# Optimization experiments

Measured on AMD Instinct MI355X. Metric: run time of the kernel, lower is better.

Reference implementation:

```python
import jax, jax.numpy as jnp
import numpy as np

B, IN, H, U = 65536, 128, 256, 256

def lecun_tanh(x):
    return 1.7159 * jnp.tanh(0.666 * x)

def _xavier(key, shape):
    fan_out, fan_in = shape
    limit = np.sqrt(6.0 / (fan_in + fan_out))
    return jax.random.uniform(key, shape, jnp.float32, -limit, limit)

def setup_inputs() -> dict:
    key = jax.random.key(0)
    ks = jax.random.split(key, 12)
    return {
        "input": jax.random.normal(ks[0], (B, IN), jnp.float32),
        "hx": jax.random.normal(ks[1], (B, H), jnp.float32),
        "ts": jax.random.uniform(ks[2], (B, 1), jnp.float32),
        # backbone Linear(IN+H -> U)
        "Wb": _xavier(ks[3], (U, IN + H)),
        "bb": jnp.zeros((U,), jnp.float32),
        # ff1, ff2, time_a, time_b: Linear(U -> H)
        "W1": _xavier(ks[4], (H, U)),
        "b1": jnp.zeros((H,), jnp.float32),
        "W2": _xavier(ks[5], (H, U)),
        "b2": jnp.zeros((H,), jnp.float32),
        "Wa": _xavier(ks[6], (H, U)),
        "ba": jnp.zeros((H,), jnp.float32),
        "Wt": _xavier(ks[7], (H, U)),
        "bt": jnp.zeros((H,), jnp.float32),
    }

def reference(input, hx, ts, Wb, bb, W1, b1, W2, b2, Wa, ba, Wt, bt):
    # x = cat([input, hx]) -> backbone MLP (1 layer, LeCun tanh)
    x = jnp.concatenate([input, hx], axis=1)          # [B, IN+H]
    x = lecun_tanh(x @ Wb.T + bb)                     # [B, U]
    ff1 = jnp.tanh(x @ W1.T + b1)                     # [B, H]
    ff2 = jnp.tanh(x @ W2.T + b2)
    t_a = x @ Wa.T + ba
    t_b = x @ Wt.T + bt
    t_interp = jax.nn.sigmoid(t_a * ts + t_b)         # ts broadcasts [B,1]
    new_hidden = ff1 * (1.0 - t_interp) + t_interp * ff2
    return new_hidden
```

## Files before the change

kernel.cpp:

```cpp
#include <hip/hip_runtime.h>

typedef float v4f __attribute__((ext_vector_type(4)));
typedef short v8s __attribute__((ext_vector_type(8)));

#define BM 64

__device__ __forceinline__ unsigned short f2bf(float f) {
    union { float f; unsigned u; } v; v.f = f;
    unsigned u = v.u;
    u += 0x7FFFu + ((u >> 16) & 1u);
    return (unsigned short)(u >> 16);
}

__device__ __forceinline__ unsigned cvt_pk_bf16(float lo, float hi) {
    unsigned r;
    asm("v_cvt_pk_bf16_f32 %0, %1, %2" : "=v"(r) : "v"(lo), "v"(hi));
    return r;
}

__device__ __forceinline__ void gload_lds16(const unsigned short* g, unsigned short* l) {
    __builtin_amdgcn_global_load_lds(
        (const __attribute__((address_space(1))) void*)(const void*)g,
        (__attribute__((address_space(3))) void*)(void*)l,
        16, 0, 0);
}

#define LDS_BARRIER() do {                                        \
    asm volatile("s_waitcnt lgkmcnt(0)" ::: "memory");            \
    __builtin_amdgcn_s_barrier();                                 \
    __builtin_amdgcn_sched_barrier(0);                            \
} while (0)

__device__ __forceinline__ float fast_exp2(float x) {
#if __has_builtin(__builtin_amdgcn_exp2f)
    return __builtin_amdgcn_exp2f(x);
#else
    return exp2f(x);
#endif
}
__device__ __forceinline__ float fast_rcp(float x) {
#if __has_builtin(__builtin_amdgcn_rcpf)
    return __builtin_amdgcn_rcpf(x);
#else
    return 1.0f / x;
#endif
}
__device__ __forceinline__ float fast_tanh(float y) {
    float t = fast_exp2(y * 2.885390081777927f);
    return (t - 1.0f) * fast_rcp(t + 1.0f);
}
__device__ __forceinline__ float fast_sigmoid(float z) {
    float t = fast_exp2(-1.4426950408889634f * z);
    return fast_rcp(1.0f + t);
}

__global__ void prep_pack(const float* __restrict__ Wb, const float* __restrict__ W1,
                          const float* __restrict__ W2, const float* __restrict__ Wa,
                          const float* __restrict__ Wt, unsigned short* __restrict__ ws)
{
    int e = blockIdx.x * 256 + threadIdx.x;
    if (e >= 360448) return;
    const float* src; int K; int base;
    if (e < 98304)       { src = Wb; K = 384; base = 0; }
    else if (e < 163840) { src = W1; K = 256; base = 98304; }
    else if (e < 229376) { src = W2; K = 256; base = 163840; }
    else if (e < 294912) { src = Wa; K = 256; base = 229376; }
    else                 { src = Wt; K = 256; base = 294912; }
    int le   = e - base;
    int j    = le & 7;
    int lane = (le >> 3) & 63;
    int tile = le >> 9;
    int kt   = K >> 5;
    int ks   = tile % kt;
    int nt   = tile / kt;
    int n = nt * 16 + (lane & 15);
    int k = ks * 32 + (lane >> 4) * 8 + j;
    ws[e] = f2bf(src[n * K + k]);
}

__global__ __launch_bounds__(256, 2) void cfc_fused(
    const float* __restrict__ xin, const float* __restrict__ hx,
    const float* __restrict__ ts,
    const float* __restrict__ bb, const float* __restrict__ b1,
    const float* __restrict__ b2, const float* __restrict__ ba,
    const float* __restrict__ bt,
    const unsigned short* __restrict__ wpk,
    float* __restrict__ out)
{
    __shared__ unsigned short lds[40960];
    const int tid  = threadIdx.x;
    const int lane = tid & 63;
    const int w    = tid >> 6;
    const int row0 = blockIdx.x * BM;

    auto STAGE = [&](int s) {
        unsigned short* wb = &lds[16384 + (s % 3) * 8192 + w * 2048];
        #pragma unroll
        for (int i = 0; i < 4; ++i) {
            size_t goff;
            if (s < 12) {
                goff = (size_t)((w * 4 + i) * 12 + s) * 512;
            } else {
                int s2 = s - 12, g = s2 >> 3, ks = s2 & 7;
                goff = 98304u + (size_t)i * 65536
                     + (size_t)((w * 4 + g) * 8 + ks) * 512;
            }
            gload_lds16(wpk + goff + (size_t)lane * 8, wb + i * 512);
        }
    };

    STAGE(0); STAGE(1);

    v4f acc[4][4];
    #pragma unroll
    for (int nt = 0; nt < 4; ++nt) {
        float bv = bb[w * 64 + nt * 16 + (lane & 15)];
        v4f bvv = {bv, bv, bv, bv};
        #pragma unroll
        for (int mt = 0; mt < 4; ++mt) acc[nt][mt] = bvv;
    }

    #pragma unroll 1
    for (int c = 0; c < 3; ++c) {
        const float* src = (c == 0) ? (xin + (size_t)row0 * 128)
                                    : (hx + (size_t)row0 * 256 + (c == 2 ? 128 : 0));
        const int srcld = (c == 0) ? 128 : 256;
        v4f stg[8];
        #pragma unroll
        for (int it = 0; it < 8; ++it) {
            int i  = tid + it * 256;
            int r  = i >> 5;
            int c4 = i & 31;
            stg[it] = *(reinterpret_cast<const v4f*>(src + (size_t)r * srcld) + c4);
        }
        LDS_BARRIER();
        #pragma unroll
        for (int it = 0; it < 8; ++it) {
            int i  = tid + it * 256;
            int r  = i >> 5;
            int c4 = i & 31;
            uint2 pk;
            pk.x = cvt_pk_bf16(stg[it][0], stg[it][1]);
            pk.y = cvt_pk_bf16(stg[it][2], stg[it][3]);
            int idx = (((r >> 4) * 4 + (c4 >> 3)) * 64 + ((c4 >> 1) & 3) * 16 + (r & 15)) * 8
                      + (c4 & 1) * 4;
            *reinterpret_cast<uint2*>(&lds[idx]) = pk;
        }
        LDS_BARRIER();

        #pragma unroll 1
        for (int ksl = 0; ksl < 4; ++ksl) {
            const int s = c * 4 + ksl;
            STAGE(s + 2);
            asm volatile("s_waitcnt vmcnt(8)" ::: "memory");
            v8s a[4];
            #pragma unroll
            for (int mt = 0; mt < 4; ++mt)
                a[mt] = *reinterpret_cast<const v8s*>(&lds[((mt*4 + ksl)*64 + lane)*8]);
            const unsigned short* wb = &lds[16384 + (s % 3) * 8192 + w * 2048];
            v8s bf[4];
            #pragma unroll
            for (int nt = 0; nt < 4; ++nt)
                bf[nt] = *reinterpret_cast<const v8s*>(wb + nt * 512 + lane * 8);
            #pragma unroll
            for (int nt = 0; nt < 4; ++nt)
                #pragma unroll
                for (int mt = 0; mt < 4; ++mt)
                    acc[nt][mt] = __builtin_amdgcn_mfma_f32_16x16x32_bf16(a[mt], bf[nt], acc[nt][mt], 0, 0, 0);
        }
    }

    float tsh[4][4];
    #pragma unroll
    for (int mt = 0; mt < 4; ++mt)
        #pragma unroll
        for (int r = 0; r < 4; ++r)
            tsh[mt][r] = ts[row0 + mt*16 + ((lane >> 4) << 2) + r];

    LDS_BARRIER();

    #pragma unroll
    for (int nt = 0; nt < 4; ++nt)
        #pragma unroll
        for (int mt = 0; mt < 4; ++mt)
            #pragma unroll
            for (int r = 0; r < 4; ++r) {
                float xv = 1.7159f * fast_tanh(0.666f * acc[nt][mt][r]);
                int idx = ((mt*8 + w*2 + (nt >> 1)) * 64
                           + ((nt & 1)*2 + ((lane >> 3) & 1)) * 16 + (lane >> 4)*4 + r) * 8
                          + (lane & 7);
                lds[idx] = f2bf(xv);
            }
    LDS_BARRIER();

    #pragma unroll 1
    for (int g = 0; g < 4; ++g) {
        const int n = w * 64 + g * 16 + (lane & 15);
        v4f a2[4][4];
        {
            float v1 = b1[n], v2 = b2[n], va = ba[n], vt = bt[n];
            v4f q1 = {v1,v1,v1,v1}, q2 = {v2,v2,v2,v2}, qa = {va,va,va,va}, qt = {vt,vt,vt,vt};
            #pragma unroll
            for (int mt = 0; mt < 4; ++mt) {
                a2[0][mt] = q1; a2[1][mt] = q2; a2[2][mt] = qa; a2[3][mt] = qt;
            }
        }
        #pragma unroll 1
        for (int ks = 0; ks < 8; ++ks) {
            const int s = 12 + g * 8 + ks;
            if (s <= 41) {
                STAGE(s + 2);
                asm volatile("s_waitcnt vmcnt(8)" ::: "memory");
            } else if (s == 42) {
                asm volatile("s_waitcnt vmcnt(4)" ::: "memory");
            } else {
                asm volatile("s_waitcnt vmcnt(0)" ::: "memory");
            }
            v8s a[4];
            #pragma unroll
            for (int mt = 0; mt < 4; ++mt)
                a[mt] = *reinterpret_cast<const v8s*>(&lds[((mt*8 + ks)*64 + lane)*8]);
            const unsigned short* wb = &lds[16384 + (s % 3) * 8192 + w * 2048];
            v8s bf[4];
            #pragma unroll
            for (int mat = 0; mat < 4; ++mat)
                bf[mat] = *reinterpret_cast<const v8s*>(wb + mat * 512 + lane * 8);
            #pragma unroll
            for (int mat = 0; mat < 4; ++mat)
                #pragma unroll
                for (int mt = 0; mt < 4; ++mt)
                    a2[mat][mt] = __builtin_amdgcn_mfma_f32_16x16x32_bf16(a[mt], bf[mat], a2[mat][mt], 0, 0, 0);
        }
        #pragma unroll
        for (int mt = 0; mt < 4; ++mt) {
            int rowb = row0 + mt*16 + ((lane >> 4) << 2);
            #pragma unroll
            for (int r = 0; r < 4; ++r) {
                float ff1 = fast_tanh(a2[0][mt][r]);
                float ff2 = fast_tanh(a2[1][mt][r]);
                float ti  = fast_sigmoid(a2[2][mt][r] * tsh[mt][r] + a2[3][mt][r]);
                out[(size_t)(rowb + r) * 256 + n] = ff1 + ti * (ff2 - ff1);
            }
        }
    }
}

extern "C" void kernel_launch(void* const* d_in, const int* in_sizes, int n_in,
                              void* d_out, int out_size, void* d_ws, size_t ws_size,
                              hipStream_t stream)
{
    const float* xin = (const float*)d_in[0];
    const float* hx  = (const float*)d_in[1];
    const float* ts  = (const float*)d_in[2];
    const float* Wb  = (const float*)d_in[3];
    const float* bb  = (const float*)d_in[4];
    const float* W1  = (const float*)d_in[5];
    const float* b1  = (const float*)d_in[6];
    const float* W2  = (const float*)d_in[7];
    const float* b2  = (const float*)d_in[8];
    const float* Wa  = (const float*)d_in[9];
    const float* ba  = (const float*)d_in[10];
    const float* Wt  = (const float*)d_in[11];
    const float* bt  = (const float*)d_in[12];

    if (ws_size < 360448 * sizeof(unsigned short)) return;
    unsigned short* wpk = (unsigned short*)d_ws;

    prep_pack<<<1408, 256, 0, stream>>>(Wb, W1, W2, Wa, Wt, wpk);
    cfc_fused<<<1024, 256, 0, stream>>>(xin, hx, ts, bb, b1, b2, ba, bt, wpk,
                                        (float*)d_out);
}
```

Measured before the change: 79.09 us.

## Double-buffer LDS fragments in register for second GEMM and raise MFMA priority

The second GEMM loop now prefetches the next k-step's A and B fragments from LDS into a second set of registers while the current step's MFMAs run. To make that possible, the vmcnt wait is tightened so the following stage is already resident. In the first GEMM, A-fragment reads move ahead of the global-load wait. Both loops wrap their MFMA blocks in s_setprio to favour matrix issue across waves. The intent is to hide LDS read latency behind MFMA work, at the cost of more VGPRs and a tighter dependence on the global-to-LDS staging order.

```diff
diff --git a/kernel.cpp b/kernel.cpp
--- a/kernel.cpp
+++ b/kernel.cpp
@@ -152,21 +152,23 @@
         for (int ksl = 0; ksl < 4; ++ksl) {
             const int s = c * 4 + ksl;
             STAGE(s + 2);
-            asm volatile("s_waitcnt vmcnt(8)" ::: "memory");
             v8s a[4];
             #pragma unroll
             for (int mt = 0; mt < 4; ++mt)
                 a[mt] = *reinterpret_cast<const v8s*>(&lds[((mt*4 + ksl)*64 + lane)*8]);
+            asm volatile("s_waitcnt vmcnt(8)" ::: "memory");
             const unsigned short* wb = &lds[16384 + (s % 3) * 8192 + w * 2048];
             v8s bf[4];
             #pragma unroll
             for (int nt = 0; nt < 4; ++nt)
                 bf[nt] = *reinterpret_cast<const v8s*>(wb + nt * 512 + lane * 8);
+            __builtin_amdgcn_s_setprio(1);
             #pragma unroll
             for (int nt = 0; nt < 4; ++nt)
                 #pragma unroll
                 for (int mt = 0; mt < 4; ++mt)
                     acc[nt][mt] = __builtin_amdgcn_mfma_f32_16x16x32_bf16(a[mt], bf[nt], acc[nt][mt], 0, 0, 0);
+            __builtin_amdgcn_s_setprio(0);
         }
     }
 
@@ -192,6 +194,46 @@
                 lds[idx] = f2bf(xv);
             }
     LDS_BARRIER();
+
+    v8s afA[4], bfA[4], afB[4], bfB[4];
+
+    auto STEP = [&](v8s (&afC)[4], v8s (&bfC)[4], v8s (&afP)[4], v8s (&bfP)[4],
+                    v4f (&a2)[4][4], int g, int ks) {
+        const int s = 12 + g * 8 + ks;
+        if (s <= 41) {
+            STAGE(s + 2);
+            asm volatile("s_waitcnt vmcnt(4)" ::: "memory");
+        } else {
+            asm volatile("s_waitcnt vmcnt(0)" ::: "memory");
+        }
+        const int nks = (ks + 1) & 7;
+        const int sn  = (s < 43) ? (s + 1) : s;
+        #pragma unroll
+        for (int mt = 0; mt < 4; ++mt)
+            afP[mt] = *reinterpret_cast<const v8s*>(&lds[((mt*8 + nks)*64 + lane)*8]);
+        const unsigned short* wbp = &lds[16384 + (sn % 3) * 8192 + w * 2048];
+        #pragma unroll
+        for (int mat = 0; mat < 4; ++mat)
+            bfP[mat] = *reinterpret_cast<const v8s*>(wbp + mat * 512 + lane * 8);
+        __builtin_amdgcn_s_setprio(1);
+        #pragma unroll
+        for (int mat = 0; mat < 4; ++mat)
+            #pragma unroll
+            for (int mt = 0; mt < 4; ++mt)
+                a2[mat][mt] = __builtin_amdgcn_mfma_f32_16x16x32_bf16(afC[mt], bfC[mat], a2[mat][mt], 0, 0, 0);
+        __builtin_amdgcn_s_setprio(0);
+    };
+
+    asm volatile("s_waitcnt vmcnt(4)" ::: "memory");
+    #pragma unroll
+    for (int mt = 0; mt < 4; ++mt)
+        afA[mt] = *reinterpret_cast<const v8s*>(&lds[((mt*8 + 0)*64 + lane)*8]);
+    {
+        const unsigned short* wb = &lds[16384 + 0 * 8192 + w * 2048];
+        #pragma unroll
+        for (int mat = 0; mat < 4; ++mat)
+            bfA[mat] = *reinterpret_cast<const v8s*>(wb + mat * 512 + lane * 8);
+    }
 
     #pragma unroll 1
     for (int g = 0; g < 4; ++g) {
@@ -206,30 +248,9 @@
             }
         }
         #pragma unroll 1
-        for (int ks = 0; ks < 8; ++ks) {
-            const int s = 12 + g * 8 + ks;
-            if (s <= 41) {
-                STAGE(s + 2);
-                asm volatile("s_waitcnt vmcnt(8)" ::: "memory");
-            } else if (s == 42) {
-                asm volatile("s_waitcnt vmcnt(4)" ::: "memory");
-            } else {
-                asm volatile("s_waitcnt vmcnt(0)" ::: "memory");
-            }
-            v8s a[4];
-            #pragma unroll
-            for (int mt = 0; mt < 4; ++mt)
-                a[mt] = *reinterpret_cast<const v8s*>(&lds[((mt*8 + ks)*64 + lane)*8]);
-            const unsigned short* wb = &lds[16384 + (s % 3) * 8192 + w * 2048];
-            v8s bf[4];
-            #pragma unroll
-            for (int mat = 0; mat < 4; ++mat)
-                bf[mat] = *reinterpret_cast<const v8s*>(wb + mat * 512 + lane * 8);
-            #pragma unroll
-            for (int mat = 0; mat < 4; ++mat)
-                #pragma unroll
-                for (int mt = 0; mt < 4; ++mt)
-                    a2[mat][mt] = __builtin_amdgcn_mfma_f32_16x16x32_bf16(a[mt], bf[mat], a2[mat][mt], 0, 0, 0);
+        for (int kp = 0; kp < 4; ++kp) {
+            STEP(afA, bfA, afB, bfB, a2, g, kp * 2);
+            STEP(afB, bfB, afA, bfA, a2, g, kp * 2 + 1);
         }
         #pragma unroll
         for (int mt = 0; mt < 4; ++mt) {
```

Result: slower. 82.95 us (+4.9%).

## Fully unroll kernel phases, prefetch next input chunk, cache A fragments in registers

Applied to the files above, without the earlier changes.

Unrolls both GEMM phases into macro steps with explicit vmcnt waits and issues the global loads for the next input chunk (hx halves) before the current chunk's MFMAs run. This overlaps input fetch with compute instead of stalling at each chunk. It also hoists the phase-2 A fragments into registers once, raises wave priority around MFMA bursts, and vectorizes the ts load. The cost is higher register pressure (two staging buffers plus 32 A fragments), which could reduce occupancy or cause spills, and the hand-tuned vmcnt counts must match the issued load order exactly.

```diff
diff --git a/kernel.cpp b/kernel.cpp
--- a/kernel.cpp
+++ b/kernel.cpp
@@ -24,6 +24,8 @@
         (__attribute__((address_space(3))) void*)(void*)l,
         16, 0, 0);
 }
+
+#define VMW(N) asm volatile("s_waitcnt vmcnt(" #N ")" ::: "memory")
 
 #define LDS_BARRIER() do {                                        \
     asm volatile("s_waitcnt lgkmcnt(0)" ::: "memory");            \
@@ -109,6 +111,96 @@
         }
     };
 
+#define ISSUE_IN(SRC, LD, BUF) do {                                           \
+    _Pragma("unroll")                                                         \
+    for (int it = 0; it < 8; ++it) {                                          \
+        int i_ = tid + it * 256; int r_ = i_ >> 5; int c4_ = i_ & 31;         \
+        BUF[it] = *(reinterpret_cast<const v4f*>((SRC) + (size_t)r_ * (LD)) + c4_); \
+    }                                                                         \
+} while (0)
+
+#define WRITE_IN(BUF) do {                                                    \
+    _Pragma("unroll")                                                         \
+    for (int it = 0; it < 8; ++it) {                                          \
+        int i_ = tid + it * 256; int r_ = i_ >> 5; int c4_ = i_ & 31;         \
+        uint2 pk_;                                                            \
+        pk_.x = cvt_pk_bf16(BUF[it][0], BUF[it][1]);                          \
+        pk_.y = cvt_pk_bf16(BUF[it][2], BUF[it][3]);                          \
+        int idx_ = (((r_ >> 4) * 4 + (c4_ >> 3)) * 64 + ((c4_ >> 1) & 3) * 16 \
+                    + (r_ & 15)) * 8 + (c4_ & 1) * 4;                         \
+        *reinterpret_cast<uint2*>(&lds[idx_]) = pk_;                          \
+    }                                                                         \
+} while (0)
+
+#define P1STEP(S, N) do {                                                     \
+    STAGE((S) + 2);                                                           \
+    v8s aa_[4];                                                               \
+    _Pragma("unroll")                                                         \
+    for (int mt = 0; mt < 4; ++mt)                                            \
+        aa_[mt] = *reinterpret_cast<const v8s*>(                              \
+                      &lds[((mt * 4 + ((S) & 3)) * 64 + lane) * 8]);          \
+    VMW(N);                                                                   \
+    const unsigned short* wb_ = &lds[16384 + ((S) % 3) * 8192 + w * 2048];    \
+    v8s bf_[4];                                                               \
+    _Pragma("unroll")                                                         \
+    for (int nt = 0; nt < 4; ++nt)                                            \
+        bf_[nt] = *reinterpret_cast<const v8s*>(wb_ + nt * 512 + lane * 8);   \
+    __builtin_amdgcn_s_setprio(1);                                            \
+    _Pragma("unroll")                                                         \
+    for (int nt = 0; nt < 4; ++nt)                                            \
+        _Pragma("unroll")                                                     \
+        for (int mt = 0; mt < 4; ++mt)                                        \
+            acc[nt][mt] = __builtin_amdgcn_mfma_f32_16x16x32_bf16(            \
+                              aa_[mt], bf_[nt], acc[nt][mt], 0, 0, 0);        \
+    __builtin_amdgcn_s_setprio(0);                                            \
+} while (0)
+
+#define P2BODY(S, KS, N) do {                                                 \
+    VMW(N);                                                                   \
+    const unsigned short* wb_ = &lds[16384 + ((S) % 3) * 8192 + w * 2048];    \
+    v8s bf_[4];                                                               \
+    _Pragma("unroll")                                                         \
+    for (int mat = 0; mat < 4; ++mat)                                         \
+        bf_[mat] = *reinterpret_cast<const v8s*>(wb_ + mat * 512 + lane * 8); \
+    __builtin_amdgcn_s_setprio(1);                                            \
+    _Pragma("unroll")                                                         \
+    for (int mat = 0; mat < 4; ++mat)                                         \
+        _Pragma("unroll")                                                     \
+        for (int mt = 0; mt < 4; ++mt)                                        \
+            a2[mat][mt] = __builtin_amdgcn_mfma_f32_16x16x32_bf16(            \
+                              afr[mt][(KS)], bf_[mat], a2[mat][mt], 0, 0, 0); \
+    __builtin_amdgcn_s_setprio(0);                                            \
+} while (0)
+
+#define P2STEP(S, KS, N)    do { STAGE((S) + 2); P2BODY(S, KS, N); } while (0)
+#define P2STEP_NS(S, KS, N) do { P2BODY(S, KS, N); } while (0)
+
+#define GINIT(G) do {                                                         \
+    const int n_ = w * 64 + (G) * 16 + (lane & 15);                           \
+    float v1_ = b1[n_], v2_ = b2[n_], va_ = ba[n_], vt_ = bt[n_];             \
+    v4f q1_ = {v1_,v1_,v1_,v1_}, q2_ = {v2_,v2_,v2_,v2_};                     \
+    v4f qa_ = {va_,va_,va_,va_}, qt_ = {vt_,vt_,vt_,vt_};                     \
+    _Pragma("unroll")                                                         \
+    for (int mt = 0; mt < 4; ++mt) {                                          \
+        a2[0][mt] = q1_; a2[1][mt] = q2_; a2[2][mt] = qa_; a2[3][mt] = qt_;   \
+    }                                                                         \
+} while (0)
+
+#define EPI(G) do {                                                           \
+    const int n_ = w * 64 + (G) * 16 + (lane & 15);                           \
+    _Pragma("unroll")                                                         \
+    for (int mt = 0; mt < 4; ++mt) {                                          \
+        int rowb_ = row0 + mt * 16 + ((lane >> 4) << 2);                      \
+        _Pragma("unroll")                                                     \
+        for (int r = 0; r < 4; ++r) {                                         \
+            float ff1_ = fast_tanh(a2[0][mt][r]);                             \
+            float ff2_ = fast_tanh(a2[1][mt][r]);                             \
+            float ti_  = fast_sigmoid(a2[2][mt][r] * tsv4[mt][r] + a2[3][mt][r]); \
+            out[(size_t)(rowb_ + r) * 256 + n_] = ff1_ + ti_ * (ff2_ - ff1_); \
+        }                                                                     \
+    }                                                                         \
+} while (0)
+
     STAGE(0); STAGE(1);
 
     v4f acc[4][4];
@@ -120,62 +212,30 @@
         for (int mt = 0; mt < 4; ++mt) acc[nt][mt] = bvv;
     }
 
-    #pragma unroll 1
-    for (int c = 0; c < 3; ++c) {
-        const float* src = (c == 0) ? (xin + (size_t)row0 * 128)
-                                    : (hx + (size_t)row0 * 256 + (c == 2 ? 128 : 0));
-        const int srcld = (c == 0) ? 128 : 256;
-        v4f stg[8];
-        #pragma unroll
-        for (int it = 0; it < 8; ++it) {
-            int i  = tid + it * 256;
-            int r  = i >> 5;
-            int c4 = i & 31;
-            stg[it] = *(reinterpret_cast<const v4f*>(src + (size_t)r * srcld) + c4);
-        }
-        LDS_BARRIER();
-        #pragma unroll
-        for (int it = 0; it < 8; ++it) {
-            int i  = tid + it * 256;
-            int r  = i >> 5;
-            int c4 = i & 31;
-            uint2 pk;
-            pk.x = cvt_pk_bf16(stg[it][0], stg[it][1]);
-            pk.y = cvt_pk_bf16(stg[it][2], stg[it][3]);
-            int idx = (((r >> 4) * 4 + (c4 >> 3)) * 64 + ((c4 >> 1) & 3) * 16 + (r & 15)) * 8
-                      + (c4 & 1) * 4;
-            *reinterpret_cast<uint2*>(&lds[idx]) = pk;
-        }
-        LDS_BARRIER();
-
-        #pragma unroll 1
-        for (int ksl = 0; ksl < 4; ++ksl) {
-            const int s = c * 4 + ksl;
-            STAGE(s + 2);
-            asm volatile("s_waitcnt vmcnt(8)" ::: "memory");
-            v8s a[4];
-            #pragma unroll
-            for (int mt = 0; mt < 4; ++mt)
-                a[mt] = *reinterpret_cast<const v8s*>(&lds[((mt*4 + ksl)*64 + lane)*8]);
-            const unsigned short* wb = &lds[16384 + (s % 3) * 8192 + w * 2048];
-            v8s bf[4];
-            #pragma unroll
-            for (int nt = 0; nt < 4; ++nt)
-                bf[nt] = *reinterpret_cast<const v8s*>(wb + nt * 512 + lane * 8);
-            #pragma unroll
-            for (int nt = 0; nt < 4; ++nt)
-                #pragma unroll
-                for (int mt = 0; mt < 4; ++mt)
-                    acc[nt][mt] = __builtin_amdgcn_mfma_f32_16x16x32_bf16(a[mt], bf[nt], acc[nt][mt], 0, 0, 0);
-        }
-    }
-
-    float tsh[4][4];
+    v4f stgA[8], stgB[8];
+    ISSUE_IN(xin + (size_t)row0 * 128, 128, stgA);
+    VMW(0);
+    WRITE_IN(stgA);
+    ISSUE_IN(hx + (size_t)row0 * 256, 256, stgB);
+    LDS_BARRIER();
+    P1STEP(0, 16); P1STEP(1, 16); P1STEP(2, 8); P1STEP(3, 8);
+    LDS_BARRIER();
+    VMW(16);
+    WRITE_IN(stgB);
+    ISSUE_IN(hx + (size_t)row0 * 256 + 128, 256, stgA);
+    LDS_BARRIER();
+    P1STEP(4, 16); P1STEP(5, 16); P1STEP(6, 8); P1STEP(7, 8);
+    LDS_BARRIER();
+    VMW(16);
+    WRITE_IN(stgA);
+    LDS_BARRIER();
+    P1STEP(8, 8); P1STEP(9, 8); P1STEP(10, 8); P1STEP(11, 8);
+
+    v4f tsv4[4];
     #pragma unroll
     for (int mt = 0; mt < 4; ++mt)
-        #pragma unroll
-        for (int r = 0; r < 4; ++r)
-            tsh[mt][r] = ts[row0 + mt*16 + ((lane >> 4) << 2) + r];
+        tsv4[mt] = *reinterpret_cast<const v4f*>(
+                       &ts[row0 + mt * 16 + ((lane >> 4) << 2)]);
 
     LDS_BARRIER();
 
@@ -193,56 +253,40 @@
             }
     LDS_BARRIER();
 
-    #pragma unroll 1
-    for (int g = 0; g < 4; ++g) {
-        const int n = w * 64 + g * 16 + (lane & 15);
-        v4f a2[4][4];
-        {
-            float v1 = b1[n], v2 = b2[n], va = ba[n], vt = bt[n];
-            v4f q1 = {v1,v1,v1,v1}, q2 = {v2,v2,v2,v2}, qa = {va,va,va,va}, qt = {vt,vt,vt,vt};
-            #pragma unroll
-            for (int mt = 0; mt < 4; ++mt) {
-                a2[0][mt] = q1; a2[1][mt] = q2; a2[2][mt] = qa; a2[3][mt] = qt;
-            }
-        }
-        #pragma unroll 1
-        for (int ks = 0; ks < 8; ++ks) {
-            const int s = 12 + g * 8 + ks;
-            if (s <= 41) {
-                STAGE(s + 2);
-                asm volatile("s_waitcnt vmcnt(8)" ::: "memory");
-            } else if (s == 42) {
-                asm volatile("s_waitcnt vmcnt(4)" ::: "memory");
-            } else {
-                asm volatile("s_waitcnt vmcnt(0)" ::: "memory");
-            }
-            v8s a[4];
-            #pragma unroll
-            for (int mt = 0; mt < 4; ++mt)
-                a[mt] = *reinterpret_cast<const v8s*>(&lds[((mt*8 + ks)*64 + lane)*8]);
-            const unsigned short* wb = &lds[16384 + (s % 3) * 8192 + w * 2048];
-            v8s bf[4];
-            #pragma unroll
-            for (int mat = 0; mat < 4; ++mat)
-                bf[mat] = *reinterpret_cast<const v8s*>(wb + mat * 512 + lane * 8);
-            #pragma unroll
-            for (int mat = 0; mat < 4; ++mat)
-                #pragma unroll
-                for (int mt = 0; mt < 4; ++mt)
-                    a2[mat][mt] = __builtin_amdgcn_mfma_f32_16x16x32_bf16(a[mt], bf[mat], a2[mat][mt], 0, 0, 0);
-        }
+    v8s afr[4][8];
+    #pragma unroll
+    for (int mt = 0; mt < 4; ++mt)
         #pragma unroll
-        for (int mt = 0; mt < 4; ++mt) {
-            int rowb = row0 + mt*16 + ((lane >> 4) << 2);
-            #pragma unroll
-            for (int r = 0; r < 4; ++r) {
-                float ff1 = fast_tanh(a2[0][mt][r]);
-                float ff2 = fast_tanh(a2[1][mt][r]);
-                float ti  = fast_sigmoid(a2[2][mt][r] * tsh[mt][r] + a2[3][mt][r]);
-                out[(size_t)(rowb + r) * 256 + n] = ff1 + ti * (ff2 - ff1);
-            }
-        }
-    }
+        for (int ks = 0; ks < 8; ++ks)
+            afr[mt][ks] = *reinterpret_cast<const v8s*>(
+                              &lds[((mt * 8 + ks) * 64 + lane) * 8]);
+
+    v4f a2[4][4];
+    GINIT(0);
+    P2STEP(12,0,16); P2STEP(13,1,16); P2STEP(14,2,8); P2STEP(15,3,8);
+    P2STEP(16,4,8);  P2STEP(17,5,8);  P2STEP(18,6,8); P2STEP(19,7,8);
+    EPI(0);
+    GINIT(1);
+    P2STEP(20,0,28); P2STEP(21,1,28); P2STEP(22,2,8); P2STEP(23,3,8);
+    P2STEP(24,4,8);  P2STEP(25,5,8);  P2STEP(26,6,8); P2STEP(27,7,8);
+    EPI(1);
+    GINIT(2);
+    P2STEP(28,0,28); P2STEP(29,1,28); P2STEP(30,2,8); P2STEP(31,3,8);
+    P2STEP(32,4,8);  P2STEP(33,5,8);  P2STEP(34,6,8); P2STEP(35,7,8);
+    EPI(2);
+    GINIT(3);
+    P2STEP(36,0,28); P2STEP(37,1,28); P2STEP(38,2,8); P2STEP(39,3,8);
+    P2STEP(40,4,8);  P2STEP(41,5,8);  P2STEP_NS(42,6,4); P2STEP_NS(43,7,0);
+    EPI(3);
+
+#undef ISSUE_IN
+#undef WRITE_IN
+#undef P1STEP
+#undef P2BODY
+#undef P2STEP
+#undef P2STEP_NS
+#undef GINIT
+#undef EPI
 }
 
 extern "C" void kernel_launch(void* const* d_in, const int* in_sizes, int n_in,
```

New measurement: 85.74 us. 1.08x slower.
